# Performance work log

Hardware: AMD Instinct MI355X
Metric: run time of the kernel (lower is better)

## Reference

```python
import jax, jax.numpy as jnp
import numpy as np

N, E, IN_DIM, OUT_DIM, T = 100000, 1600000, 128, 64, 8
V_THRESHOLD = 1.0
EPS = 1e-7

# ---- Lorentz manifold (curvature -1), time coordinate first ----

def _linner(a, b):
    # Lorentzian inner product <a,b>_L = -a0*b0 + sum_i ai*bi
    return -a[..., 0] * b[..., 0] + jnp.sum(a[..., 1:] * b[..., 1:], axis=-1)

def _proju(z, u):
    # project ambient vector u to tangent space at z (<z,z>_L = -1)
    return u + _linner(z, u)[..., None] * z

def _expmap(z, u):
    un = jnp.sqrt(jnp.maximum(_linner(u, u), EPS))[..., None]
    return jnp.cosh(un) * z + jnp.sinh(un) * u / un

def _dist0(z):
    # geodesic distance to origin o=(1,0,...,0): arccosh(-<o,z>_L) = arccosh(z0)
    return jnp.arccosh(jnp.maximum(z[..., 0], 1.0 + EPS))

# ---- GCNConv (torch_geometric semantics: self-loops + symmetric norm) ----

def _gcn(x, edge_index, W, b):
    src, dst = edge_index[0], edge_index[1]
    loops = jnp.arange(N, dtype=src.dtype)
    src = jnp.concatenate([src, loops])
    dst = jnp.concatenate([dst, loops])
    deg = jax.ops.segment_sum(jnp.ones_like(dst, dtype=x.dtype), dst, num_segments=N)
    dinv = jax.lax.rsqrt(jnp.maximum(deg, 1.0))  # deg >= 1 due to self-loops
    norm = dinv[src] * dinv[dst]                 # [E+N]
    h = x @ W                                    # [N, OUT_DIM]
    out = jax.ops.segment_sum(norm[:, None] * h[src], dst, num_segments=N)
    return out + b


def setup_inputs() -> dict:
    key = jax.random.key(0)
    k1, k2, k3 = jax.random.split(key, 3)
    x = jax.random.normal(k1, (N, IN_DIM), dtype=jnp.float32)
    edge_index = jax.random.randint(k2, (2, E), 0, N, dtype=jnp.int32)
    W = jax.random.normal(k3, (IN_DIM, OUT_DIM), dtype=jnp.float32) / np.sqrt(IN_DIM)
    b = jnp.zeros((OUT_DIM,), dtype=jnp.float32)
    return {"x": x, "edge_index": edge_index, "W": W, "b": b}


def reference(x, edge_index, W, b):
    h = _gcn(x, edge_index, W, b)                       # [N, D]
    origin = jnp.zeros_like(h).at[..., 0].set(1.0)      # manifold origin
    x_seq = jnp.broadcast_to(h, (T,) + h.shape)         # [T, N, D]

    def step(z, x_t):
        u = _proju(z, x_t)                              # input current in T_z M
        z_new = _expmap(z, u)                           # charge along geodesic
        v = _dist0(z_new)                               # membrane potential [N]
        spike = v >= V_THRESHOLD
        z_out = jnp.where(spike[..., None], origin, z_new)  # hard reset
        return z_out, (spike.astype(h.dtype), z_out)

    _, (o_seq, z_seq) = jax.lax.scan(step, origin, x_seq)
    return o_seq, z_seq  # [T, N], [T, N, D]
```

## Files before the change

### kernel.cpp

```cpp
#include <hip/hip_runtime.h>
#include <math.h>

#define IN_DIM_C 128
#define OUT_DIM_C 64
#define T_STEPS 8
#define KC_MAX 512
#define PTILE 2048
#define GKC 32

__device__ __forceinline__ float4 f4zero() { return make_float4(0.f, 0.f, 0.f, 0.f); }

__global__ __launch_bounds__(256) void k_hist(const int* __restrict__ dst,
                                              int* __restrict__ chist, int E) {
    __shared__ int hh[KC_MAX];
    const int tid = threadIdx.x;
    for (int i = tid; i < KC_MAX; i += 256) hh[i] = 0;
    __syncthreads();
    long base = (long)blockIdx.x * 4096;
    #pragma unroll
    for (int j = 0; j < 16; ++j) {
        long e = base + j * 256 + tid;
        if (e < E) atomicAdd(&hh[dst[e] >> 8], 1);
    }
    __syncthreads();
    for (int i = tid; i < KC_MAX; i += 256)
        if (hh[i]) atomicAdd(&chist[i], hh[i]);
}

__global__ __launch_bounds__(64) void k_scanK(const int* __restrict__ chist,
                                              int* __restrict__ gcursor,
                                              int* __restrict__ offsets,
                                              int kc, int n, int E) {
    int lane = threadIdx.x;
    int carry = 0;
    for (int c = 0; c * 64 < kc; ++c) {
        int idx = c * 64 + lane;
        int v = (idx < kc) ? chist[idx] : 0;
        int x = v;
        #pragma unroll
        for (int off = 1; off < 64; off <<= 1) {
            int t = __shfl_up(x, off, 64);
            if (lane >= off) x += t;
        }
        if (idx < kc) gcursor[idx] = carry + x - v;
        carry += __shfl(x, 63, 64);
    }
    if (lane == 0) offsets[n] = E;
}

__global__ __launch_bounds__(256) void k_gemm(const float* __restrict__ x,
                                              const float* __restrict__ W,
                                              float* __restrict__ h, int n) {
    __shared__ __align__(16) float xs[GKC * 132];
    __shared__ __align__(16) float Ws[GKC * OUT_DIM_C];

    const int tid = threadIdx.x;
    const int cg = tid & 7;
    const int ng = tid >> 3;
    const int node_base = blockIdx.x * 128;

    float acc[4][8];
    #pragma unroll
    for (int i = 0; i < 4; ++i)
        #pragma unroll
        for (int j = 0; j < 8; ++j) acc[i][j] = 0.f;

    #pragma unroll 1
    for (int c = 0; c < IN_DIM_C / GKC; ++c) {
        __syncthreads();
        #pragma unroll
        for (int i = 0; i < 4; ++i) {
            int idx = tid + i * 256;
            int nd = idx >> 3, k4 = idx & 7;
            int node = node_base + nd;
            float4 v = f4zero();
            if (node < n) v = *(const float4*)&x[(long)node * IN_DIM_C + c * GKC + k4 * 4];
            xs[(k4 * 4 + 0) * 132 + nd] = v.x;
            xs[(k4 * 4 + 1) * 132 + nd] = v.y;
            xs[(k4 * 4 + 2) * 132 + nd] = v.z;
            xs[(k4 * 4 + 3) * 132 + nd] = v.w;
        }
        #pragma unroll
        for (int i = 0; i < 2; ++i) {
            int idx = tid + i * 256;
            ((float4*)Ws)[idx] = ((const float4*)&W[c * GKC * OUT_DIM_C])[idx];
        }
        __syncthreads();

        #pragma unroll
        for (int k = 0; k < GKC; ++k) {
            float4 a = *(const float4*)&xs[k * 132 + ng * 4];
            const float* wr = &Ws[k * OUT_DIM_C + cg * 8];
            float4 b0 = *(const float4*)&wr[0];
            float4 b1 = *(const float4*)&wr[4];
            #pragma unroll
            for (int i = 0; i < 4; ++i) {
                float av = (i == 0) ? a.x : (i == 1) ? a.y : (i == 2) ? a.z : a.w;
                acc[i][0] = fmaf(av, b0.x, acc[i][0]);
                acc[i][1] = fmaf(av, b0.y, acc[i][1]);
                acc[i][2] = fmaf(av, b0.z, acc[i][2]);
                acc[i][3] = fmaf(av, b0.w, acc[i][3]);
                acc[i][4] = fmaf(av, b1.x, acc[i][4]);
                acc[i][5] = fmaf(av, b1.y, acc[i][5]);
                acc[i][6] = fmaf(av, b1.z, acc[i][6]);
                acc[i][7] = fmaf(av, b1.w, acc[i][7]);
            }
        }
    }

    #pragma unroll
    for (int i = 0; i < 4; ++i) {
        int node = node_base + ng * 4 + i;
        if (node < n) {
            *(float4*)&h[(long)node * OUT_DIM_C + cg * 8] =
                make_float4(acc[i][0], acc[i][1], acc[i][2], acc[i][3]);
            *(float4*)&h[(long)node * OUT_DIM_C + cg * 8 + 4] =
                make_float4(acc[i][4], acc[i][5], acc[i][6], acc[i][7]);
        }
    }
}

__global__ __launch_bounds__(256) void k_part(const int* __restrict__ src,
                                              const int* __restrict__ dst,
                                              int* __restrict__ gcursor,
                                              int* __restrict__ part, int E, int kc) {
    __shared__ int hist[KC_MAX];
    __shared__ int offs[KC_MAX];
    __shared__ int cur[KC_MAX];
    __shared__ int gbase[KC_MAX];
    const int tid = threadIdx.x;
    long base = (long)blockIdx.x * PTILE;

    for (int i = tid; i < KC_MAX; i += 256) hist[i] = 0;
    __syncthreads();
    #pragma unroll
    for (int j = 0; j < PTILE / 256; ++j) {
        long e = base + j * 256 + tid;
        if (e < E) atomicAdd(&hist[dst[e] >> 8], 1);
    }
    __syncthreads();
    if (tid < 64) {
        int carry = 0;
        for (int c = 0; c * 64 < kc; ++c) {
            int idx = c * 64 + tid;
            int v = (idx < kc) ? hist[idx] : 0;
            int x = v;
            #pragma unroll
            for (int off = 1; off < 64; off <<= 1) {
                int t = __shfl_up(x, off, 64);
                if (tid >= off) x += t;
            }
            if (idx < kc) { offs[idx] = carry + x - v; cur[idx] = carry + x - v; }
            carry += __shfl(x, 63, 64);
        }
    }
    __syncthreads();
    for (int b = tid; b < kc; b += 256)
        gbase[b] = hist[b] ? atomicAdd(&gcursor[b], hist[b]) : 0;
    __syncthreads();
    #pragma unroll
    for (int j = 0; j < PTILE / 256; ++j) {
        long e = base + j * 256 + tid;
        if (e < E) {
            int d = dst[e];
            int b = d >> 8;
            int r = atomicAdd(&cur[b], 1);
            part[gbase[b] + r - offs[b]] = (src[e] << 8) | (d & 255);
        }
    }
}

__global__ __launch_bounds__(256) void k_sort(const int* __restrict__ part,
                                              const int* __restrict__ gcursor,
                                              int* __restrict__ part2,
                                              int* __restrict__ offsets,
                                              float* __restrict__ dinv, int n) {
    __shared__ int cnt[256];
    __shared__ int cur[256];
    __shared__ int wsum[4], woff[4];
    const int tid = threadIdx.x;
    const int bkt = blockIdx.x;
    int start = bkt ? gcursor[bkt - 1] : 0;
    int end = gcursor[bkt];

    cnt[tid] = 0;
    __syncthreads();
    for (int i = start + tid; i < end; i += 256)
        atomicAdd(&cnt[part[i] & 255], 1);
    __syncthreads();

    int v = cnt[tid];
    int lane = tid & 63, wv = tid >> 6;
    int x = v;
    #pragma unroll
    for (int off = 1; off < 64; off <<= 1) {
        int t = __shfl_up(x, off, 64);
        if (lane >= off) x += t;
    }
    if (lane == 63) wsum[wv] = x;
    __syncthreads();
    if (tid == 0) { int c = 0; for (int w = 0; w < 4; ++w) { woff[w] = c; c += wsum[w]; } }
    __syncthreads();
    int myloc = woff[wv] + x - v;
    cur[tid] = myloc;
    int node = (bkt << 8) + tid;
    if (node < n) {
        offsets[node] = start + myloc;
        dinv[node] = rsqrtf((float)(v + 1));
    }
    __syncthreads();

    for (int i = start + tid; i < end; i += 256) {
        int p = part[i];
        int r = atomicAdd(&cur[p & 255], 1);
        part2[start + r] = ((unsigned)p) >> 8;
    }
}

__global__ __launch_bounds__(256) void k_pullspike(const int* __restrict__ offsets,
                                                   const int* __restrict__ part2,
                                                   const float* __restrict__ dinv,
                                                   const float* __restrict__ h,
                                                   const float* __restrict__ b,
                                                   float* __restrict__ o_seq,
                                                   float* __restrict__ z_seq, int n) {
    int gid = blockIdx.x * 256 + threadIdx.x;
    int node = gid >> 4;
    int sub = threadIdx.x & 15;
    if (node >= n) return;
    const float s0 = (sub == 0) ? -1.0f : 1.0f;
    int lane0 = (threadIdx.x & 63) & ~15;

    int o0 = offsets[node], o1 = offsets[node + 1];
    float dd = dinv[node];
    float4 hv = *(const float4*)&h[(long)node * OUT_DIM_C + sub * 4];
    float4 bv = *(const float4*)&b[sub * 4];
    float dd2 = dd * dd;
    float4 g = make_float4(fmaf(dd2, hv.x, bv.x), fmaf(dd2, hv.y, bv.y),
                           fmaf(dd2, hv.z, bv.z), fmaf(dd2, hv.w, bv.w));
    int i = o0;
    for (; i + 4 <= o1; i += 4) {
        int s0i = part2[i], s1i = part2[i + 1], s2i = part2[i + 2], s3i = part2[i + 3];
        float w0 = dinv[s0i] * dd, w1 = dinv[s1i] * dd;
        float w2 = dinv[s2i] * dd, w3 = dinv[s3i] * dd;
        float4 h0 = *(const float4*)&h[(long)s0i * OUT_DIM_C + sub * 4];
        float4 h1 = *(const float4*)&h[(long)s1i * OUT_DIM_C + sub * 4];
        float4 h2 = *(const float4*)&h[(long)s2i * OUT_DIM_C + sub * 4];
        float4 h3 = *(const float4*)&h[(long)s3i * OUT_DIM_C + sub * 4];
        g.x = fmaf(w0, h0.x, g.x); g.y = fmaf(w0, h0.y, g.y);
        g.z = fmaf(w0, h0.z, g.z); g.w = fmaf(w0, h0.w, g.w);
        g.x = fmaf(w1, h1.x, g.x); g.y = fmaf(w1, h1.y, g.y);
        g.z = fmaf(w1, h1.z, g.z); g.w = fmaf(w1, h1.w, g.w);
        g.x = fmaf(w2, h2.x, g.x); g.y = fmaf(w2, h2.y, g.y);
        g.z = fmaf(w2, h2.z, g.z); g.w = fmaf(w2, h2.w, g.w);
        g.x = fmaf(w3, h3.x, g.x); g.y = fmaf(w3, h3.y, g.y);
        g.z = fmaf(w3, h3.z, g.z); g.w = fmaf(w3, h3.w, g.w);
    }
    for (; i < o1; ++i) {
        int s = part2[i];
        float w = dinv[s] * dd;
        float4 h0 = *(const float4*)&h[(long)s * OUT_DIM_C + sub * 4];
        g.x = fmaf(w, h0.x, g.x); g.y = fmaf(w, h0.y, g.y);
        g.z = fmaf(w, h0.z, g.z); g.w = fmaf(w, h0.w, g.w);
    }

    float4 origin = f4zero();
    if (sub == 0) origin.x = 1.0f;

    auto step = [&](float4 z, float4& zn, bool& sp) {
        float p = s0 * z.x * g.x + z.y * g.y + z.z * g.z + z.w * g.w;
        p += __shfl_xor(p, 1, 64);
        p += __shfl_xor(p, 2, 64);
        p += __shfl_xor(p, 4, 64);
        p += __shfl_xor(p, 8, 64);
        float4 u = make_float4(fmaf(p, z.x, g.x), fmaf(p, z.y, g.y),
                               fmaf(p, z.z, g.z), fmaf(p, z.w, g.w));
        float q = s0 * u.x * u.x + u.y * u.y + u.z * u.z + u.w * u.w;
        q += __shfl_xor(q, 1, 64);
        q += __shfl_xor(q, 2, 64);
        q += __shfl_xor(q, 4, 64);
        q += __shfl_xor(q, 8, 64);
        float un = sqrtf(fmaxf(q, 1e-7f));
        float c = coshf(un);
        float sh = sinhf(un) / un;
        zn = make_float4(fmaf(c, z.x, sh * u.x), fmaf(c, z.y, sh * u.y),
                         fmaf(c, z.z, sh * u.z), fmaf(c, z.w, sh * u.w));
        float z0 = __shfl(zn.x, lane0, 64);
        float v = acoshf(fmaxf(z0, 1.0f + 1e-7f));
        sp = (v >= 1.0f);
    };

    float4 z1; bool sp0;
    step(origin, z1, sp0);
    float4 r0 = sp0 ? origin : z1;

    float4 z = origin;
    bool at0 = true;
    for (int t = 0; t < T_STEPS; ++t) {
        float4 zn; bool sp;
        if (at0) { sp = sp0; zn = r0; }
        else {
            step(z, zn, sp);
            if (sp) zn = origin;
        }
        *(float4*)&z_seq[(long)t * n * OUT_DIM_C + (long)node * OUT_DIM_C + sub * 4] = zn;
        if (sub == 0) o_seq[(long)t * n + node] = sp ? 1.0f : 0.0f;
        z = zn;
        at0 = sp;
    }
}

__global__ __launch_bounds__(256) void k_pull(const int* __restrict__ offsets,
                                              const int* __restrict__ part2,
                                              const float* __restrict__ dinv,
                                              const float* __restrict__ h,
                                              const float* __restrict__ b,
                                              float* __restrict__ agg, int n) {
    int node = (blockIdx.x * 256 + threadIdx.x) >> 6;
    int lane = threadIdx.x & 63;
    if (node >= n) return;
    int o0 = offsets[node], o1 = offsets[node + 1];
    float dd = dinv[node];
    float acc = fmaf(dd * dd, h[(long)node * OUT_DIM_C + lane], b[lane]);
    int i = o0;
    for (; i + 4 <= o1; i += 4) {
        int s0 = part2[i], s1 = part2[i + 1], s2 = part2[i + 2], s3 = part2[i + 3];
        float n0 = dinv[s0] * dd, n1 = dinv[s1] * dd, n2 = dinv[s2] * dd, n3 = dinv[s3] * dd;
        acc = fmaf(n0, h[(long)s0 * OUT_DIM_C + lane], acc);
        acc = fmaf(n1, h[(long)s1 * OUT_DIM_C + lane], acc);
        acc = fmaf(n2, h[(long)s2 * OUT_DIM_C + lane], acc);
        acc = fmaf(n3, h[(long)s3 * OUT_DIM_C + lane], acc);
    }
    for (; i < o1; ++i) {
        int s = part2[i];
        acc = fmaf(dinv[s] * dd, h[(long)s * OUT_DIM_C + lane], acc);
    }
    agg[(long)node * OUT_DIM_C + lane] = acc;
}

__global__ __launch_bounds__(256) void k_spike(const float* agg,
                                               float* o_seq, float* z_seq, int n) {
    int gid = blockIdx.x * 256 + threadIdx.x;
    int node = gid >> 4;
    int sub = threadIdx.x & 15;
    if (node >= n) return;
    const float s0 = (sub == 0) ? -1.0f : 1.0f;
    int lane0 = (threadIdx.x & 63) & ~15;

    float4 g = *(const float4*)&agg[(long)node * OUT_DIM_C + sub * 4];
    float4 origin = f4zero();
    if (sub == 0) origin.x = 1.0f;

    auto step = [&](float4 z, float4& zn, bool& sp) {
        float p = s0 * z.x * g.x + z.y * g.y + z.z * g.z + z.w * g.w;
        p += __shfl_xor(p, 1, 64);
        p += __shfl_xor(p, 2, 64);
        p += __shfl_xor(p, 4, 64);
        p += __shfl_xor(p, 8, 64);
        float4 u = make_float4(fmaf(p, z.x, g.x), fmaf(p, z.y, g.y),
                               fmaf(p, z.z, g.z), fmaf(p, z.w, g.w));
        float q = s0 * u.x * u.x + u.y * u.y + u.z * u.z + u.w * u.w;
        q += __shfl_xor(q, 1, 64);
        q += __shfl_xor(q, 2, 64);
        q += __shfl_xor(q, 4, 64);
        q += __shfl_xor(q, 8, 64);
        float un = sqrtf(fmaxf(q, 1e-7f));
        float c = coshf(un);
        float sh = sinhf(un) / un;
        zn = make_float4(fmaf(c, z.x, sh * u.x), fmaf(c, z.y, sh * u.y),
                         fmaf(c, z.z, sh * u.z), fmaf(c, z.w, sh * u.w));
        float z0 = __shfl(zn.x, lane0, 64);
        float v = acoshf(fmaxf(z0, 1.0f + 1e-7f));
        sp = (v >= 1.0f);
    };

    float4 z1; bool sp0;
    step(origin, z1, sp0);
    float4 r0 = sp0 ? origin : z1;

    float4 z = origin;
    bool at0 = true;
    for (int t = 0; t < T_STEPS; ++t) {
        float4 zn; bool sp;
        if (at0) { sp = sp0; zn = r0; }
        else {
            step(z, zn, sp);
            if (sp) zn = origin;
        }
        *(float4*)&z_seq[(long)t * n * OUT_DIM_C + (long)node * OUT_DIM_C + sub * 4] = zn;
        if (sub == 0) o_seq[(long)t * n + node] = sp ? 1.0f : 0.0f;
        z = zn;
        at0 = sp;
    }
}

static inline size_t align256(size_t x) { return (x + 255) & ~(size_t)255; }

extern "C" void kernel_launch(void* const* d_in, const int* in_sizes, int n_in,
                              void* d_out, int out_size, void* d_ws, size_t ws_size,
                              hipStream_t stream) {
    const float* x  = (const float*)d_in[0];
    const int*   ei = (const int*)d_in[1];
    const float* W  = (const float*)d_in[2];
    const float* b  = (const float*)d_in[3];
    const int N = in_sizes[0] / IN_DIM_C;
    const int E = in_sizes[1] / 2;
    const int KC = (N + 255) >> 8;

    float* out   = (float*)d_out;
    float* o_seq = out;
    float* z_seq = out + (long)T_STEPS * N;

    const int* srcp = ei;
    const int* dstp = ei + E;

    size_t off_h    = 0;
    size_t off_p2   = align256(off_h + (size_t)N * OUT_DIM_C * 4);
    size_t off_offs = align256(off_p2 + (size_t)E * 4);
    size_t off_dinv = align256(off_offs + (size_t)(N + 1) * 4);
    size_t need     = align256(off_dinv + (size_t)N * 4);

    if (d_ws != nullptr && ws_size >= need) {
        float* h       = (float*)((char*)d_ws + off_h);
        int*   part2   = (int*)((char*)d_ws + off_p2);
        int*   offsets = (int*)((char*)d_ws + off_offs);
        float* dinv    = (float*)((char*)d_ws + off_dinv);
        int*   part    = (int*)(z_seq + 0L * N * OUT_DIM_C);
        int*   chist   = (int*)(z_seq + 1L * N * OUT_DIM_C);
        int*   gcursor = chist + KC_MAX;

        hipMemsetAsync(chist, 0, (size_t)KC_MAX * sizeof(int), stream);
        k_hist<<<(E + 4095) / 4096, 256, 0, stream>>>(dstp, chist, E);
        k_scanK<<<1, 64, 0, stream>>>(chist, gcursor, offsets, KC, N, E);

        k_gemm<<<(N + 127) / 128, 256, 0, stream>>>(x, W, h, N);

        k_part<<<(E + PTILE - 1) / PTILE, 256, 0, stream>>>(srcp, dstp, gcursor, part, E, KC);
        k_sort<<<KC, 256, 0, stream>>>(part, gcursor, part2, offsets, dinv, N);

        k_pullspike<<<(N + 15) / 16, 256, 0, stream>>>(offsets, part2, dinv, h, b,
                                                       o_seq, z_seq, N);
    } else {
        float* agg     = z_seq;
        float* h       = z_seq + 1L * N * OUT_DIM_C;
        int*   part    = (int*)(z_seq + 2L * N * OUT_DIM_C);
        int*   part2   = (int*)(z_seq + 3L * N * OUT_DIM_C);
        int*   chist   = (int*)(z_seq + 4L * N * OUT_DIM_C);
        int*   gcursor = chist + KC_MAX;
        int*   offsets = gcursor + KC_MAX;
        float* dinv    = (float*)(offsets + N + 1);

        hipMemsetAsync(chist, 0, (size_t)KC_MAX * sizeof(int), stream);
        k_hist<<<(E + 4095) / 4096, 256, 0, stream>>>(dstp, chist, E);
        k_scanK<<<1, 64, 0, stream>>>(chist, gcursor, offsets, KC, N, E);

        k_gemm<<<(N + 127) / 128, 256, 0, stream>>>(x, W, h, N);

        k_part<<<(E + PTILE - 1) / PTILE, 256, 0, stream>>>(srcp, dstp, gcursor, part, E, KC);
        k_sort<<<KC, 256, 0, stream>>>(part, gcursor, part2, offsets, dinv, N);
        k_pull<<<(N * 64 + 255) / 256, 256, 0, stream>>>(offsets, part2, dinv, h, b, agg, N);

        k_spike<<<(N + 15) / 16, 256, 0, stream>>>(agg, o_seq, z_seq, N);
    }
}
```

Before: 405.2 us.

## Fuse GEMM with degree histogram and replace two-pass sort with atomic scatter

The GEMM and the edge histogram now run as one launch, with block ranges split between the two roles, and the histogram also builds a per-node degree array with global atomics. CSR construction then uses a per-bucket prefix scan over node degrees plus a direct scatter that claims a slot through a global atomic cursor per destination. This replaces the partition and in-bucket sort passes and removes one intermediate array round trip and some launches. In exchange it adds many global atomics on random addresses, and neighbor order within a node becomes nondeterministic, so floating-point summation order can vary between runs.

```diff
diff --git a/kernel.cpp b/kernel.cpp
--- a/kernel.cpp
+++ b/kernel.cpp
@@ -9,23 +9,6 @@
 #define GKC 32
 
 __device__ __forceinline__ float4 f4zero() { return make_float4(0.f, 0.f, 0.f, 0.f); }
-
-__global__ __launch_bounds__(256) void k_hist(const int* __restrict__ dst,
-                                              int* __restrict__ chist, int E) {
-    __shared__ int hh[KC_MAX];
-    const int tid = threadIdx.x;
-    for (int i = tid; i < KC_MAX; i += 256) hh[i] = 0;
-    __syncthreads();
-    long base = (long)blockIdx.x * 4096;
-    #pragma unroll
-    for (int j = 0; j < 16; ++j) {
-        long e = base + j * 256 + tid;
-        if (e < E) atomicAdd(&hh[dst[e] >> 8], 1);
-    }
-    __syncthreads();
-    for (int i = tid; i < KC_MAX; i += 256)
-        if (hh[i]) atomicAdd(&chist[i], hh[i]);
-}
 
 __global__ __launch_bounds__(64) void k_scanK(const int* __restrict__ chist,
                                               int* __restrict__ gcursor,
@@ -48,148 +31,114 @@
     if (lane == 0) offsets[n] = E;
 }
 
-__global__ __launch_bounds__(256) void k_gemm(const float* __restrict__ x,
-                                              const float* __restrict__ W,
-                                              float* __restrict__ h, int n) {
-    __shared__ __align__(16) float xs[GKC * 132];
-    __shared__ __align__(16) float Ws[GKC * OUT_DIM_C];
-
-    const int tid = threadIdx.x;
-    const int cg = tid & 7;
-    const int ng = tid >> 3;
-    const int node_base = blockIdx.x * 128;
-
-    float acc[4][8];
-    #pragma unroll
-    for (int i = 0; i < 4; ++i)
-        #pragma unroll
-        for (int j = 0; j < 8; ++j) acc[i][j] = 0.f;
-
-    #pragma unroll 1
-    for (int c = 0; c < IN_DIM_C / GKC; ++c) {
-        __syncthreads();
-        #pragma unroll
-        for (int i = 0; i < 4; ++i) {
-            int idx = tid + i * 256;
-            int nd = idx >> 3, k4 = idx & 7;
-            int node = node_base + nd;
-            float4 v = f4zero();
-            if (node < n) v = *(const float4*)&x[(long)node * IN_DIM_C + c * GKC + k4 * 4];
-            xs[(k4 * 4 + 0) * 132 + nd] = v.x;
-            xs[(k4 * 4 + 1) * 132 + nd] = v.y;
-            xs[(k4 * 4 + 2) * 132 + nd] = v.z;
-            xs[(k4 * 4 + 3) * 132 + nd] = v.w;
-        }
-        #pragma unroll
-        for (int i = 0; i < 2; ++i) {
-            int idx = tid + i * 256;
-            ((float4*)Ws)[idx] = ((const float4*)&W[c * GKC * OUT_DIM_C])[idx];
-        }
-        __syncthreads();
-
-        #pragma unroll
-        for (int k = 0; k < GKC; ++k) {
-            float4 a = *(const float4*)&xs[k * 132 + ng * 4];
-            const float* wr = &Ws[k * OUT_DIM_C + cg * 8];
-            float4 b0 = *(const float4*)&wr[0];
-            float4 b1 = *(const float4*)&wr[4];
+__global__ __launch_bounds__(256) void k_gemm_hist(const float* __restrict__ x,
+                                                   const float* __restrict__ W,
+                                                   float* __restrict__ h,
+                                                   const int* __restrict__ dst,
+                                                   int* __restrict__ chist,
+                                                   int* __restrict__ deg,
+                                                   int n, int E, int gemm_blocks) {
+    __shared__ __align__(16) float smem[GKC * 132 + GKC * OUT_DIM_C];
+
+    if ((int)blockIdx.x < gemm_blocks) {
+        float* xs = smem;
+        float* Ws = smem + GKC * 132;
+        const int tid = threadIdx.x;
+        const int cg = tid & 7;
+        const int ng = tid >> 3;
+        const int node_base = blockIdx.x * 128;
+
+        float acc[4][8];
+        #pragma unroll
+        for (int i = 0; i < 4; ++i)
+            #pragma unroll
+            for (int j = 0; j < 8; ++j) acc[i][j] = 0.f;
+
+        #pragma unroll 1
+        for (int c = 0; c < IN_DIM_C / GKC; ++c) {
+            __syncthreads();
             #pragma unroll
             for (int i = 0; i < 4; ++i) {
-                float av = (i == 0) ? a.x : (i == 1) ? a.y : (i == 2) ? a.z : a.w;
-                acc[i][0] = fmaf(av, b0.x, acc[i][0]);
-                acc[i][1] = fmaf(av, b0.y, acc[i][1]);
-                acc[i][2] = fmaf(av, b0.z, acc[i][2]);
-                acc[i][3] = fmaf(av, b0.w, acc[i][3]);
-                acc[i][4] = fmaf(av, b1.x, acc[i][4]);
-                acc[i][5] = fmaf(av, b1.y, acc[i][5]);
-                acc[i][6] = fmaf(av, b1.z, acc[i][6]);
-                acc[i][7] = fmaf(av, b1.w, acc[i][7]);
+                int idx = tid + i * 256;
+                int nd = idx >> 3, k4 = idx & 7;
+                int node = node_base + nd;
+                float4 v = f4zero();
+                if (node < n) v = *(const float4*)&x[(long)node * IN_DIM_C + c * GKC + k4 * 4];
+                xs[(k4 * 4 + 0) * 132 + nd] = v.x;
+                xs[(k4 * 4 + 1) * 132 + nd] = v.y;
+                xs[(k4 * 4 + 2) * 132 + nd] = v.z;
+                xs[(k4 * 4 + 3) * 132 + nd] = v.w;
             }
-        }
-    }
-
-    #pragma unroll
-    for (int i = 0; i < 4; ++i) {
-        int node = node_base + ng * 4 + i;
-        if (node < n) {
-            *(float4*)&h[(long)node * OUT_DIM_C + cg * 8] =
-                make_float4(acc[i][0], acc[i][1], acc[i][2], acc[i][3]);
-            *(float4*)&h[(long)node * OUT_DIM_C + cg * 8 + 4] =
-                make_float4(acc[i][4], acc[i][5], acc[i][6], acc[i][7]);
-        }
-    }
-}
-
-__global__ __launch_bounds__(256) void k_part(const int* __restrict__ src,
-                                              const int* __restrict__ dst,
-                                              int* __restrict__ gcursor,
-                                              int* __restrict__ part, int E, int kc) {
-    __shared__ int hist[KC_MAX];
-    __shared__ int offs[KC_MAX];
-    __shared__ int cur[KC_MAX];
-    __shared__ int gbase[KC_MAX];
-    const int tid = threadIdx.x;
-    long base = (long)blockIdx.x * PTILE;
-
-    for (int i = tid; i < KC_MAX; i += 256) hist[i] = 0;
-    __syncthreads();
-    #pragma unroll
-    for (int j = 0; j < PTILE / 256; ++j) {
-        long e = base + j * 256 + tid;
-        if (e < E) atomicAdd(&hist[dst[e] >> 8], 1);
-    }
-    __syncthreads();
-    if (tid < 64) {
-        int carry = 0;
-        for (int c = 0; c * 64 < kc; ++c) {
-            int idx = c * 64 + tid;
-            int v = (idx < kc) ? hist[idx] : 0;
-            int x = v;
             #pragma unroll
-            for (int off = 1; off < 64; off <<= 1) {
-                int t = __shfl_up(x, off, 64);
-                if (tid >= off) x += t;
+            for (int i = 0; i < 2; ++i) {
+                int idx = tid + i * 256;
+                ((float4*)Ws)[idx] = ((const float4*)&W[c * GKC * OUT_DIM_C])[idx];
             }
-            if (idx < kc) { offs[idx] = carry + x - v; cur[idx] = carry + x - v; }
-            carry += __shfl(x, 63, 64);
-        }
-    }
-    __syncthreads();
-    for (int b = tid; b < kc; b += 256)
-        gbase[b] = hist[b] ? atomicAdd(&gcursor[b], hist[b]) : 0;
-    __syncthreads();
-    #pragma unroll
-    for (int j = 0; j < PTILE / 256; ++j) {
-        long e = base + j * 256 + tid;
-        if (e < E) {
-            int d = dst[e];
-            int b = d >> 8;
-            int r = atomicAdd(&cur[b], 1);
-            part[gbase[b] + r - offs[b]] = (src[e] << 8) | (d & 255);
-        }
-    }
-}
-
-__global__ __launch_bounds__(256) void k_sort(const int* __restrict__ part,
-                                              const int* __restrict__ gcursor,
-                                              int* __restrict__ part2,
-                                              int* __restrict__ offsets,
-                                              float* __restrict__ dinv, int n) {
-    __shared__ int cnt[256];
-    __shared__ int cur[256];
+            __syncthreads();
+
+            #pragma unroll
+            for (int k = 0; k < GKC; ++k) {
+                float4 a = *(const float4*)&xs[k * 132 + ng * 4];
+                const float* wr = &Ws[k * OUT_DIM_C + cg * 8];
+                float4 b0 = *(const float4*)&wr[0];
+                float4 b1 = *(const float4*)&wr[4];
+                #pragma unroll
+                for (int i = 0; i < 4; ++i) {
+                    float av = (i == 0) ? a.x : (i == 1) ? a.y : (i == 2) ? a.z : a.w;
+                    acc[i][0] = fmaf(av, b0.x, acc[i][0]);
+                    acc[i][1] = fmaf(av, b0.y, acc[i][1]);
+                    acc[i][2] = fmaf(av, b0.z, acc[i][2]);
+                    acc[i][3] = fmaf(av, b0.w, acc[i][3]);
+                    acc[i][4] = fmaf(av, b1.x, acc[i][4]);
+                    acc[i][5] = fmaf(av, b1.y, acc[i][5]);
+                    acc[i][6] = fmaf(av, b1.z, acc[i][6]);
+                    acc[i][7] = fmaf(av, b1.w, acc[i][7]);
+                }
+            }
+        }
+
+        #pragma unroll
+        for (int i = 0; i < 4; ++i) {
+            int node = node_base + ng * 4 + i;
+            if (node < n) {
+                *(float4*)&h[(long)node * OUT_DIM_C + cg * 8] =
+                    make_float4(acc[i][0], acc[i][1], acc[i][2], acc[i][3]);
+                *(float4*)&h[(long)node * OUT_DIM_C + cg * 8 + 4] =
+                    make_float4(acc[i][4], acc[i][5], acc[i][6], acc[i][7]);
+            }
+        }
+    } else {
+        int* hh = (int*)smem;
+        const int tid = threadIdx.x;
+        int hb = blockIdx.x - gemm_blocks;
+        for (int i = tid; i < KC_MAX; i += 256) hh[i] = 0;
+        __syncthreads();
+        long base = (long)hb * 4096;
+        #pragma unroll
+        for (int j = 0; j < 16; ++j) {
+            long e = base + j * 256 + tid;
+            if (e < E) {
+                int d = dst[e];
+                atomicAdd(&hh[d >> 8], 1);
+                atomicAdd(&deg[d], 1);
+            }
+        }
+        __syncthreads();
+        for (int i = tid; i < KC_MAX; i += 256)
+            if (hh[i]) atomicAdd(&chist[i], hh[i]);
+    }
+}
+
+__global__ __launch_bounds__(256) void k_offsets(const int* __restrict__ deg,
+                                                 const int* __restrict__ gcursor,
+                                                 int* __restrict__ offsets,
+                                                 int* __restrict__ cursor,
+                                                 float* __restrict__ dinv, int n) {
     __shared__ int wsum[4], woff[4];
     const int tid = threadIdx.x;
     const int bkt = blockIdx.x;
-    int start = bkt ? gcursor[bkt - 1] : 0;
-    int end = gcursor[bkt];
-
-    cnt[tid] = 0;
-    __syncthreads();
-    for (int i = start + tid; i < end; i += 256)
-        atomicAdd(&cnt[part[i] & 255], 1);
-    __syncthreads();
-
-    int v = cnt[tid];
+    int node = (bkt << 8) + tid;
+    int v = (node < n) ? deg[node] : 0;
     int lane = tid & 63, wv = tid >> 6;
     int x = v;
     #pragma unroll
@@ -202,18 +151,27 @@
     if (tid == 0) { int c = 0; for (int w = 0; w < 4; ++w) { woff[w] = c; c += wsum[w]; } }
     __syncthreads();
     int myloc = woff[wv] + x - v;
-    cur[tid] = myloc;
-    int node = (bkt << 8) + tid;
     if (node < n) {
-        offsets[node] = start + myloc;
+        int o = gcursor[bkt] + myloc;
+        offsets[node] = o;
+        cursor[node] = o;
         dinv[node] = rsqrtf((float)(v + 1));
     }
-    __syncthreads();
-
-    for (int i = start + tid; i < end; i += 256) {
-        int p = part[i];
-        int r = atomicAdd(&cur[p & 255], 1);
-        part2[start + r] = ((unsigned)p) >> 8;
+}
+
+__global__ __launch_bounds__(256) void k_scatter(const int* __restrict__ src,
+                                                 const int* __restrict__ dst,
+                                                 int* __restrict__ cursor,
+                                                 int* __restrict__ part2, int E) {
+    long base = (long)blockIdx.x * 4096;
+    #pragma unroll
+    for (int j = 0; j < 16; ++j) {
+        long e = base + j * 256 + threadIdx.x;
+        if (e < E) {
+            int d = dst[e];
+            int r = atomicAdd(&cursor[d], 1);
+            part2[r] = src[e];
+        }
     }
 }
 
@@ -310,6 +268,192 @@
     }
 }
 
+__global__ __launch_bounds__(256) void k_hist(const int* __restrict__ dst,
+                                              int* __restrict__ chist, int E) {
+    __shared__ int hh[KC_MAX];
+    const int tid = threadIdx.x;
+    for (int i = tid; i < KC_MAX; i += 256) hh[i] = 0;
+    __syncthreads();
+    long base = (long)blockIdx.x * 4096;
+    #pragma unroll
+    for (int j = 0; j < 16; ++j) {
+        long e = base + j * 256 + tid;
+        if (e < E) atomicAdd(&hh[dst[e] >> 8], 1);
+    }
+    __syncthreads();
+    for (int i = tid; i < KC_MAX; i += 256)
+        if (hh[i]) atomicAdd(&chist[i], hh[i]);
+}
+
+__global__ __launch_bounds__(256) void k_gemm(const float* __restrict__ x,
+                                              const float* __restrict__ W,
+                                              float* __restrict__ h, int n) {
+    __shared__ __align__(16) float xs[GKC * 132];
+    __shared__ __align__(16) float Ws[GKC * OUT_DIM_C];
+
+    const int tid = threadIdx.x;
+    const int cg = tid & 7;
+    const int ng = tid >> 3;
+    const int node_base = blockIdx.x * 128;
+
+    float acc[4][8];
+    #pragma unroll
+    for (int i = 0; i < 4; ++i)
+        #pragma unroll
+        for (int j = 0; j < 8; ++j) acc[i][j] = 0.f;
+
+    #pragma unroll 1
+    for (int c = 0; c < IN_DIM_C / GKC; ++c) {
+        __syncthreads();
+        #pragma unroll
+        for (int i = 0; i < 4; ++i) {
+            int idx = tid + i * 256;
+            int nd = idx >> 3, k4 = idx & 7;
+            int node = node_base + nd;
+            float4 v = f4zero();
+            if (node < n) v = *(const float4*)&x[(long)node * IN_DIM_C + c * GKC + k4 * 4];
+            xs[(k4 * 4 + 0) * 132 + nd] = v.x;
+            xs[(k4 * 4 + 1) * 132 + nd] = v.y;
+            xs[(k4 * 4 + 2) * 132 + nd] = v.z;
+            xs[(k4 * 4 + 3) * 132 + nd] = v.w;
+        }
+        #pragma unroll
+        for (int i = 0; i < 2; ++i) {
+            int idx = tid + i * 256;
+            ((float4*)Ws)[idx] = ((const float4*)&W[c * GKC * OUT_DIM_C])[idx];
+        }
+        __syncthreads();
+
+        #pragma unroll
+        for (int k = 0; k < GKC; ++k) {
+            float4 a = *(const float4*)&xs[k * 132 + ng * 4];
+            const float* wr = &Ws[k * OUT_DIM_C + cg * 8];
+            float4 b0 = *(const float4*)&wr[0];
+            float4 b1 = *(const float4*)&wr[4];
+            #pragma unroll
+            for (int i = 0; i < 4; ++i) {
+                float av = (i == 0) ? a.x : (i == 1) ? a.y : (i == 2) ? a.z : a.w;
+                acc[i][0] = fmaf(av, b0.x, acc[i][0]);
+                acc[i][1] = fmaf(av, b0.y, acc[i][1]);
+                acc[i][2] = fmaf(av, b0.z, acc[i][2]);
+                acc[i][3] = fmaf(av, b0.w, acc[i][3]);
+                acc[i][4] = fmaf(av, b1.x, acc[i][4]);
+                acc[i][5] = fmaf(av, b1.y, acc[i][5]);
+                acc[i][6] = fmaf(av, b1.z, acc[i][6]);
+                acc[i][7] = fmaf(av, b1.w, acc[i][7]);
+            }
+        }
+    }
+
+    #pragma unroll
+    for (int i = 0; i < 4; ++i) {
+        int node = node_base + ng * 4 + i;
+        if (node < n) {
+            *(float4*)&h[(long)node * OUT_DIM_C + cg * 8] =
+                make_float4(acc[i][0], acc[i][1], acc[i][2], acc[i][3]);
+            *(float4*)&h[(long)node * OUT_DIM_C + cg * 8 + 4] =
+                make_float4(acc[i][4], acc[i][5], acc[i][6], acc[i][7]);
+        }
+    }
+}
+
+__global__ __launch_bounds__(256) void k_part(const int* __restrict__ src,
+                                              const int* __restrict__ dst,
+                                              int* __restrict__ gcursor,
+                                              int* __restrict__ part, int E, int kc) {
+    __shared__ int hist[KC_MAX];
+    __shared__ int offs[KC_MAX];
+    __shared__ int cur[KC_MAX];
+    __shared__ int gbase[KC_MAX];
+    const int tid = threadIdx.x;
+    long base = (long)blockIdx.x * PTILE;
+
+    for (int i = tid; i < KC_MAX; i += 256) hist[i] = 0;
+    __syncthreads();
+    #pragma unroll
+    for (int j = 0; j < PTILE / 256; ++j) {
+        long e = base + j * 256 + tid;
+        if (e < E) atomicAdd(&hist[dst[e] >> 8], 1);
+    }
+    __syncthreads();
+    if (tid < 64) {
+        int carry = 0;
+        for (int c = 0; c * 64 < kc; ++c) {
+            int idx = c * 64 + tid;
+            int v = (idx < kc) ? hist[idx] : 0;
+            int x = v;
+            #pragma unroll
+            for (int off = 1; off < 64; off <<= 1) {
+                int t = __shfl_up(x, off, 64);
+                if (tid >= off) x += t;
+            }
+            if (idx < kc) { offs[idx] = carry + x - v; cur[idx] = carry + x - v; }
+            carry += __shfl(x, 63, 64);
+        }
+    }
+    __syncthreads();
+    for (int b = tid; b < kc; b += 256)
+        gbase[b] = hist[b] ? atomicAdd(&gcursor[b], hist[b]) : 0;
+    __syncthreads();
+    #pragma unroll
+    for (int j = 0; j < PTILE / 256; ++j) {
+        long e = base + j * 256 + tid;
+        if (e < E) {
+            int d = dst[e];
+            int b = d >> 8;
+            int r = atomicAdd(&cur[b], 1);
+            part[gbase[b] + r - offs[b]] = (src[e] << 8) | (d & 255);
+        }
+    }
+}
+
+__global__ __launch_bounds__(256) void k_sort(const int* __restrict__ part,
+                                              const int* __restrict__ gcursor,
+                                              int* __restrict__ part2,
+                                              int* __restrict__ offsets,
+                                              float* __restrict__ dinv, int n) {
+    __shared__ int cnt[256];
+    __shared__ int cur[256];
+    __shared__ int wsum[4], woff[4];
+    const int tid = threadIdx.x;
+    const int bkt = blockIdx.x;
+    int start = bkt ? gcursor[bkt - 1] : 0;
+    int end = gcursor[bkt];
+
+    cnt[tid] = 0;
+    __syncthreads();
+    for (int i = start + tid; i < end; i += 256)
+        atomicAdd(&cnt[part[i] & 255], 1);
+    __syncthreads();
+
+    int v = cnt[tid];
+    int lane = tid & 63, wv = tid >> 6;
+    int x = v;
+    #pragma unroll
+    for (int off = 1; off < 64; off <<= 1) {
+        int t = __shfl_up(x, off, 64);
+        if (lane >= off) x += t;
+    }
+    if (lane == 63) wsum[wv] = x;
+    __syncthreads();
+    if (tid == 0) { int c = 0; for (int w = 0; w < 4; ++w) { woff[w] = c; c += wsum[w]; } }
+    __syncthreads();
+    int myloc = woff[wv] + x - v;
+    cur[tid] = myloc;
+    int node = (bkt << 8) + tid;
+    if (node < n) {
+        offsets[node] = start + myloc;
+        dinv[node] = rsqrtf((float)(v + 1));
+    }
+    __syncthreads();
+
+    for (int i = start + tid; i < end; i += 256) {
+        int p = part[i];
+        int r = atomicAdd(&cur[p & 255], 1);
+        part2[start + r] = ((unsigned)p) >> 8;
+    }
+}
+
 __global__ __launch_bounds__(256) void k_pull(const int* __restrict__ offsets,
                                               const int* __restrict__ part2,
                                               const float* __restrict__ dinv,
@@ -414,30 +558,35 @@
     const int* srcp = ei;
     const int* dstp = ei + E;
 
-    size_t off_h    = 0;
-    size_t off_p2   = align256(off_h + (size_t)N * OUT_DIM_C * 4);
-    size_t off_offs = align256(off_p2 + (size_t)E * 4);
-    size_t off_dinv = align256(off_offs + (size_t)(N + 1) * 4);
-    size_t need     = align256(off_dinv + (size_t)N * 4);
+    size_t off_h     = 0;
+    size_t off_p2    = align256(off_h + (size_t)N * OUT_DIM_C * 4);
+    size_t off_offs  = align256(off_p2 + (size_t)E * 4);
+    size_t off_dinv  = align256(off_offs + (size_t)(N + 1) * 4);
+    size_t off_deg   = align256(off_dinv + (size_t)N * 4);
+    size_t off_chist = align256(off_deg + (size_t)N * 4);
+    size_t off_gcur  = off_chist + (size_t)KC_MAX * 4;
+    size_t off_cur   = align256(off_gcur + (size_t)KC_MAX * 4);
+    size_t need      = align256(off_cur + (size_t)N * 4);
+
+    const int GB = (N + 127) / 128;
+    const int HB = (E + 4095) / 4096;
 
     if (d_ws != nullptr && ws_size >= need) {
         float* h       = (float*)((char*)d_ws + off_h);
         int*   part2   = (int*)((char*)d_ws + off_p2);
         int*   offsets = (int*)((char*)d_ws + off_offs);
         float* dinv    = (float*)((char*)d_ws + off_dinv);
-        int*   part    = (int*)(z_seq + 0L * N * OUT_DIM_C);
-        int*   chist   = (int*)(z_seq + 1L * N * OUT_DIM_C);
-        int*   gcursor = chist + KC_MAX;
-
-        hipMemsetAsync(chist, 0, (size_t)KC_MAX * sizeof(int), stream);
-        k_hist<<<(E + 4095) / 4096, 256, 0, stream>>>(dstp, chist, E);
+        int*   deg     = (int*)((char*)d_ws + off_deg);
+        int*   chist   = (int*)((char*)d_ws + off_chist);
+        int*   gcursor = (int*)((char*)d_ws + off_gcur);
+        int*   cursor  = (int*)((char*)d_ws + off_cur);
+
+        hipMemsetAsync(deg, 0, off_chist + (size_t)KC_MAX * 4 - off_deg, stream);
+
+        k_gemm_hist<<<GB + HB, 256, 0, stream>>>(x, W, h, dstp, chist, deg, N, E, GB);
         k_scanK<<<1, 64, 0, stream>>>(chist, gcursor, offsets, KC, N, E);
-
-        k_gemm<<<(N + 127) / 128, 256, 0, stream>>>(x, W, h, N);
-
-        k_part<<<(E + PTILE - 1) / PTILE, 256, 0, stream>>>(srcp, dstp, gcursor, part, E, KC);
-        k_sort<<<KC, 256, 0, stream>>>(part, gcursor, part2, offsets, dinv, N);
-
+        k_offsets<<<KC, 256, 0, stream>>>(deg, gcursor, offsets, cursor, dinv, N);
+        k_scatter<<<HB, 256, 0, stream>>>(srcp, dstp, cursor, part2, E);
         k_pullspike<<<(N + 15) / 16, 256, 0, stream>>>(offsets, part2, dinv, h, b,
                                                        o_seq, z_seq, N);
     } else {
@@ -451,10 +600,10 @@
         float* dinv    = (float*)(offsets + N + 1);
 
         hipMemsetAsync(chist, 0, (size_t)KC_MAX * sizeof(int), stream);
-        k_hist<<<(E + 4095) / 4096, 256, 0, stream>>>(dstp, chist, E);
+        k_hist<<<HB, 256, 0, stream>>>(dstp, chist, E);
         k_scanK<<<1, 64, 0, stream>>>(chist, gcursor, offsets, KC, N, E);
 
-        k_gemm<<<(N + 127) / 128, 256, 0, stream>>>(x, W, h, N);
+        k_gemm<<<GB, 256, 0, stream>>>(x, W, h, N);
 
         k_part<<<(E + PTILE - 1) / PTILE, 256, 0, stream>>>(srcp, dstp, gcursor, part, E, KC);
         k_sort<<<KC, 256, 0, stream>>>(part, gcursor, part2, offsets, dinv, N);
```

After: 478.8 us. 1.18x slower.
